# Performance work log

Hardware: AMD Instinct MI355X
Metric: run time of the kernel (lower is better)

## Reference

```python
import jax, jax.numpy as jnp
import numpy as np

# Dimensions (match init_kwargs / input_specs)
B, T, H, S, R, E = 4, 2048, 1024, 512, 16, 4
F = 6 + 2 * R           # engine_state_feature_dim
ETA = 0.1               # impression_rate
ACC_DECAY = 0.99        # accumulator EMA decay
EPS = 1e-6


def setup_inputs() -> dict:
    key = jax.random.key(0)
    ks = jax.random.split(key, 20)
    n = jax.random.normal
    x = n(ks[0], (B, T, H), jnp.float32)
    # ComplexLinear signal_proj: hidden -> state
    sig_Wr = n(ks[1], (H, S), jnp.float32) / np.sqrt(H).astype(np.float32)
    sig_Wi = n(ks[2], (H, S), jnp.float32) / np.sqrt(H).astype(np.float32)
    sig_br = jnp.zeros((S,), jnp.float32)
    sig_bi = jnp.zeros((S,), jnp.float32)
    # Per-engine complex state projection [E, S, R] and diagonal complex decay [E, R]
    A_r = n(ks[3], (E, S, R), jnp.float32) / np.sqrt(S).astype(np.float32)
    A_i = n(ks[4], (E, S, R), jnp.float32) / np.sqrt(S).astype(np.float32)
    mag = 0.90 + 0.09 * jax.random.uniform(ks[5], (E, R), jnp.float32)
    ph = (2.0 * np.pi) * jax.random.uniform(ks[6], (E, R), jnp.float32)
    lam_r = mag * jnp.cos(ph)
    lam_i = mag * jnp.sin(ph)
    # Per-engine ComplexLinear: feature(F) -> hidden(H)
    eh_Wr = n(ks[7], (E, F, H), jnp.float32) / np.sqrt(F).astype(np.float32)
    eh_Wi = n(ks[8], (E, F, H), jnp.float32) / np.sqrt(F).astype(np.float32)
    eh_br = jnp.zeros((E, H), jnp.float32)
    eh_bi = jnp.zeros((E, H), jnp.float32)
    # Engine fusion ComplexLinear: E*H -> H
    fu_Wr = n(ks[9], (E * H, H), jnp.float32) / np.sqrt(E * H).astype(np.float32)
    fu_Wi = n(ks[10], (E * H, H), jnp.float32) / np.sqrt(E * H).astype(np.float32)
    fu_br = jnp.zeros((H,), jnp.float32)
    fu_bi = jnp.zeros((H,), jnp.float32)
    # Gate: Linear(4H -> H)
    g_W = n(ks[11], (4 * H, H), jnp.float32) / np.sqrt(4 * H).astype(np.float32)
    g_b = jnp.zeros((H,), jnp.float32)
    return dict(x=x, sig_Wr=sig_Wr, sig_Wi=sig_Wi, sig_br=sig_br, sig_bi=sig_bi,
                A_r=A_r, A_i=A_i, lam_r=lam_r, lam_i=lam_i,
                eh_Wr=eh_Wr, eh_Wi=eh_Wi, eh_br=eh_br, eh_bi=eh_bi,
                fu_Wr=fu_Wr, fu_Wi=fu_Wi, fu_br=fu_br, fu_bi=fu_bi,
                g_W=g_W, g_b=g_b)


def _run_engines(ur, ui, lam_r, lam_i):
    """Complex diagonal recurrence over time for all engines jointly.
    ur, ui: [E,B,T,R] complex drive. Returns per-step features [E,B,T,F] (real, imag)."""
    lr = lam_r[:, None, :]  # [E,1,R]
    li = lam_i[:, None, :]

    def step(carry, u):
        hr, hi, acc = carry                      # [E,B,R], [E,B,R], [E,B]
        ur_t, ui_t = u                           # [E,B,R]
        nhr = (1.0 - ETA) * (lr * hr - li * hi) + ETA * ur_t
        nhi = (1.0 - ETA) * (lr * hi + li * hr) + ETA * ui_t
        mag2 = nhr * nhr + nhi * nhi             # [E,B,R]
        m_mean = jnp.mean(mag2, axis=-1)         # [E,B]
        nacc = ACC_DECAY * acc + (1.0 - ACC_DECAY) * m_mean
        inv = jax.lax.rsqrt(m_mean + EPS)[..., None]
        hnr, hni = nhr * inv, nhi * inv          # rms-normalized complex state
        z = jnp.zeros_like(m_mean)
        scal_r = jnp.stack([hnr.mean(-1), hni.mean(-1),
                            jnp.sqrt(m_mean + EPS),
                            jnp.sqrt(jnp.max(mag2, axis=-1) + EPS),
                            nacc, jnp.log1p(nacc)], axis=-1)   # [E,B,6]
        scal_i = jnp.stack([hni.mean(-1), -hnr.mean(-1), z, z, z, z], axis=-1)
        fr = jnp.concatenate([scal_r, hnr, hni], axis=-1)      # [E,B,F]
        fi = jnp.concatenate([scal_i, hni, -hnr], axis=-1)
        return (nhr, nhi, nacc), (fr, fi)

    init = (jnp.zeros((E, B, R), ur.dtype), jnp.zeros((E, B, R), ur.dtype),
            jnp.zeros((E, B), ur.dtype))
    u_seq = (jnp.moveaxis(ur, 2, 0), jnp.moveaxis(ui, 2, 0))   # [T,E,B,R]
    _, (frs, fis) = jax.lax.scan(step, init, u_seq)
    return jnp.moveaxis(frs, 0, 2), jnp.moveaxis(fis, 0, 2)    # [E,B,T,F]


def reference(x, sig_Wr, sig_Wi, sig_br, sig_bi, A_r, A_i, lam_r, lam_i,
              eh_Wr, eh_Wi, eh_br, eh_bi, fu_Wr, fu_Wi, fu_br, fu_bi, g_W, g_b):
    # Complex signal projection of real input: z = (Wr + i Wi)^T x + b
    zr = x @ sig_Wr + sig_br                     # [B,T,S]
    zi = x @ sig_Wi + sig_bi
    # Complex per-engine drive u = A^H-style complex matmul: [E,B,T,R]
    ur = jnp.einsum('bts,esr->ebtr', zr, A_r) - jnp.einsum('bts,esr->ebtr', zi, A_i)
    ui = jnp.einsum('bts,esr->ebtr', zr, A_i) + jnp.einsum('bts,esr->ebtr', zi, A_r)
    fr, fi = _run_engines(ur, ui, lam_r, lam_i)  # [E,B,T,F]
    # Per-engine ComplexLinear feature -> hidden
    yr = (jnp.einsum('ebtf,efh->ebth', fr, eh_Wr)
          - jnp.einsum('ebtf,efh->ebth', fi, eh_Wi)) + eh_br[:, None, None, :]
    yi = (jnp.einsum('ebtf,efh->ebth', fr, eh_Wi)
          + jnp.einsum('ebtf,efh->ebth', fi, eh_Wr)) + eh_bi[:, None, None, :]
    # Concat engines along feature axis -> [B,T,E*H]
    yr_c = jnp.moveaxis(yr, 0, 2).reshape(B, T, E * H)
    yi_c = jnp.moveaxis(yi, 0, 2).reshape(B, T, E * H)
    # Engine fusion ComplexLinear
    frf = yr_c @ fu_Wr - yi_c @ fu_Wi + fu_br    # [B,T,H]
    fif = yr_c @ fu_Wi + yi_c @ fu_Wr + fu_bi
    mag = jnp.sqrt(frf * frf + fif * fif + EPS)
    g = jax.nn.sigmoid(jnp.concatenate([x, frf, fif, mag], axis=-1) @ g_W + g_b)
    return g * frf + (1.0 - g) * x
```

## Files before the change

### kernel.cpp

```cpp
#include <hip/hip_runtime.h>
#include <stdint.h>

#define B_ 4
#define T_ 2048
#define H_ 1024
#define S_ 512
#define R_ 16
#define E_ 4
#define F_ 38
#define BT_ (B_*T_)
#define KF_ 320

typedef __attribute__((ext_vector_type(8))) __bf16 bf16x8;
typedef __attribute__((ext_vector_type(4))) float f32x4;

static __device__ __forceinline__ unsigned short f2bf(float f) {
    unsigned int u = __float_as_uint(f);
    unsigned int r = (u + 0x7fffu + ((u >> 16) & 1u)) >> 16;
    return (unsigned short)r;
}

__global__ __launch_bounds__(256) void k_gemm(
    const unsigned short* __restrict__ A, int lda,
    const unsigned short* __restrict__ BT, int ldb,
    float* __restrict__ C, int ldc,
    const float* __restrict__ bias, int K,
    size_t sA, size_t sB, size_t sC)
{
    A  += (size_t)blockIdx.z * sA;
    BT += (size_t)blockIdx.z * sB;
    C  += (size_t)blockIdx.z * sC;
    __shared__ unsigned short As[128 * 32];
    __shared__ unsigned short Bs[128 * 32];
    const int tid = threadIdx.x;
    const int l = tid & 63;
    const int w = tid >> 6;
    const int wm = w >> 1, wn = w & 1;
    const int m16 = l & 15, kg = l >> 4;
    const size_t bm = (size_t)blockIdx.y * 128;
    const size_t bn = (size_t)blockIdx.x * 128;

    const int rS = tid >> 2;
    const int kS = (tid & 3) * 8;
    const unsigned short* pA0 = A + (bm + rS) * (size_t)lda + kS;
    const unsigned short* pA1 = pA0 + (size_t)64 * lda;
    const unsigned short* pB0 = BT + (bn + rS) * (size_t)ldb + kS;
    const unsigned short* pB1 = pB0 + (size_t)64 * ldb;

    f32x4 acc[4][4];
#pragma unroll
    for (int i = 0; i < 4; ++i)
#pragma unroll
        for (int j = 0; j < 4; ++j) acc[i][j] = (f32x4){0.f, 0.f, 0.f, 0.f};

    uint4 ra0 = *(const uint4*)pA0;
    uint4 ra1 = *(const uint4*)pA1;
    uint4 rb0 = *(const uint4*)pB0;
    uint4 rb1 = *(const uint4*)pB1;

    const int s0 = tid * 8;
    const int s1 = (256 + tid) * 8;
    const int nkt = K >> 5;
    for (int kt = 0; kt < nkt; ++kt) {
        __syncthreads();
        *(uint4*)&As[s0] = ra0;
        *(uint4*)&As[s1] = ra1;
        *(uint4*)&Bs[s0] = rb0;
        *(uint4*)&Bs[s1] = rb1;
        if (kt + 1 < nkt) {
            pA0 += 32; pA1 += 32; pB0 += 32; pB1 += 32;
            ra0 = *(const uint4*)pA0;
            ra1 = *(const uint4*)pA1;
            rb0 = *(const uint4*)pB0;
            rb1 = *(const uint4*)pB1;
        }
        __syncthreads();
        bf16x8 af[4], bfr[4];
#pragma unroll
        for (int i = 0; i < 4; ++i)
            af[i] = *(const bf16x8*)&As[(wm * 64 + i * 16 + m16) * 32 + kg * 8];
#pragma unroll
        for (int j = 0; j < 4; ++j)
            bfr[j] = *(const bf16x8*)&Bs[(wn * 64 + j * 16 + m16) * 32 + kg * 8];
#pragma unroll
        for (int i = 0; i < 4; ++i)
#pragma unroll
            for (int j = 0; j < 4; ++j)
                acc[i][j] = __builtin_amdgcn_mfma_f32_16x16x32_bf16(af[i], bfr[j], acc[i][j], 0, 0, 0);
    }

#pragma unroll
    for (int j = 0; j < 4; ++j) {
        const size_t col = bn + wn * 64 + j * 16 + m16;
        const float bv = bias ? bias[col] : 0.f;
#pragma unroll
        for (int i = 0; i < 4; ++i) {
            const size_t row0 = bm + wm * 64 + i * 16 + kg * 4;
#pragma unroll
            for (int p = 0; p < 4; ++p)
                C[(row0 + p) * (size_t)ldc + col] = acc[i][j][p] + bv;
        }
    }
}

__global__ __launch_bounds__(256) void k_cast_x(const float* __restrict__ x,
                                                unsigned short* __restrict__ Abig)
{
    const int gid = blockIdx.x * 256 + threadIdx.x;
    const int row = gid >> 8;
    const int c4 = (gid & 255) << 2;
    float4 v = *(const float4*)&x[(size_t)row * H_ + c4];
    ushort4 o;
    o.x = f2bf(v.x); o.y = f2bf(v.y); o.z = f2bf(v.z); o.w = f2bf(v.w);
    *(ushort4*)&Abig[(size_t)row * 4096 + c4] = o;
}

__global__ __launch_bounds__(256) void k_gwt(const float* __restrict__ gW,
                                             unsigned short* __restrict__ gWT)
{
    __shared__ float tile[32][33];
    const int tx = threadIdx.x & 31, ty = threadIdx.x >> 5;
    const int k0 = blockIdx.x * 32, n0 = blockIdx.y * 32;
#pragma unroll
    for (int q = 0; q < 4; ++q) {
        int kk = ty * 4 + q;
        tile[kk][tx] = gW[(size_t)(k0 + kk) * H_ + n0 + tx];
    }
    __syncthreads();
#pragma unroll
    for (int q = 0; q < 4; ++q) {
        int nn = ty * 4 + q;
        gWT[(size_t)(n0 + nn) * 4096 + k0 + tx] = f2bf(tile[tx][nn]);
    }
}

__global__ __launch_bounds__(64) void k_wu(const float* __restrict__ sigWr,
                                           const float* __restrict__ sigWi,
                                           const float* __restrict__ A_r,
                                           const float* __restrict__ A_i,
                                           unsigned short* __restrict__ WuT)
{
    __shared__ float swr[S_], swi[S_];
    const int h = blockIdx.x;
    const int tid = threadIdx.x;
    for (int s = tid; s < S_; s += 64) {
        swr[s] = sigWr[(size_t)h * S_ + s];
        swi[s] = sigWi[(size_t)h * S_ + s];
    }
    __syncthreads();
    const int e = tid >> 4, r = tid & 15;
    float a0 = 0.f, a1 = 0.f;
    for (int s = 0; s < S_; ++s) {
        float ar = A_r[((size_t)(e * S_ + s)) * R_ + r];
        float ai = A_i[((size_t)(e * S_ + s)) * R_ + r];
        float wr = swr[s], wi = swi[s];
        a0 += wr * ar - wi * ai;
        a1 += wr * ai + wi * ar;
    }
    WuT[(size_t)tid * H_ + h] = f2bf(a0);
    WuT[(size_t)(64 + tid) * H_ + h] = f2bf(a1);
}

__global__ __launch_bounds__(64) void k_bu(const float* __restrict__ sigbr,
                                           const float* __restrict__ sigbi,
                                           const float* __restrict__ A_r,
                                           const float* __restrict__ A_i,
                                           float* __restrict__ b_u)
{
    const int n = blockIdx.x;
    const int lane = threadIdx.x;
    const int m = n & 63;
    const int e = m >> 4, r = m & 15;
    const bool hi = n >= 64;
    float acc = 0.f;
    for (int s = lane; s < S_; s += 64) {
        float ar = A_r[((size_t)(e * S_ + s)) * R_ + r];
        float ai = A_i[((size_t)(e * S_ + s)) * R_ + r];
        float br = sigbr[s], bi = sigbi[s];
        acc += hi ? (br * ai + bi * ar) : (br * ar - bi * ai);
    }
#pragma unroll
    for (int st = 32; st; st >>= 1) acc += __shfl_down(acc, st, 64);
    if (lane == 0) b_u[n] = acc;
}

__global__ __launch_bounds__(256) void k_prepA(const float* __restrict__ ehWr,
                                               const float* __restrict__ ehWi,
                                               const float* __restrict__ ehbr,
                                               const float* __restrict__ ehbi,
                                               unsigned short* __restrict__ Ac)
{
    const int gid = blockIdx.x * 256 + threadIdx.x;
    const int e = gid >> 16;
    const int rem = gid & 65535;
    const int row = rem >> 9;
    const int k = (rem & 511) << 2;
    float4 f = {0.f, 0.f, 0.f, 0.f};
    if (row < F_) {
        const float* src = (k < 1024) ? ehWr + ((size_t)(e * F_ + row)) * 1024 + k
                                      : ehWi + ((size_t)(e * F_ + row)) * 1024 + (k - 1024);
        f = *(const float4*)src;
    } else if (row == F_) {
        const float* src = (k < 1024) ? ehbr + (size_t)e * 1024 + k
                                      : ehbi + (size_t)e * 1024 + (k - 1024);
        f = *(const float4*)src;
    }
    ushort4 o;
    o.x = f2bf(f.x); o.y = f2bf(f.y); o.z = f2bf(f.z); o.w = f2bf(f.w);
    *(ushort4*)&Ac[(size_t)gid * 4] = o;
}

__global__ __launch_bounds__(256) void k_prepB(const float* __restrict__ fuWr,
                                               const float* __restrict__ fuWi,
                                               unsigned short* __restrict__ Bc)
{
    __shared__ float tR[32][33], tI[32][33];
    const int e = blockIdx.z;
    const int k0 = blockIdx.x * 32;
    const int h0 = blockIdx.y * 32;
    const int tx = threadIdx.x & 31, ty = threadIdx.x >> 5;
    const float* fr = fuWr + ((size_t)e * 1024 + k0) * 1024 + h0;
    const float* fi = fuWi + ((size_t)e * 1024 + k0) * 1024 + h0;
#pragma unroll
    for (int q = 0; q < 4; ++q) {
        int kk = ty * 4 + q;
        tR[kk][tx] = fr[(size_t)kk * 1024 + tx];
        tI[kk][tx] = fi[(size_t)kk * 1024 + tx];
    }
    __syncthreads();
    unsigned short* Be = Bc + (size_t)e * 2048 * 2048;
#pragma unroll
    for (int q = 0; q < 4; ++q) {
        int rr = ty * 4 + q;
        float vR = tR[tx][rr], vI = tI[tx][rr];
        size_t rowLo = (size_t)(h0 + rr) * 2048;
        size_t rowHi = (size_t)(1024 + h0 + rr) * 2048;
        Be[rowLo + k0 + tx]        = f2bf(vR);
        Be[rowLo + 1024 + k0 + tx] = f2bf(-vI);
        Be[rowHi + k0 + tx]        = f2bf(vI);
        Be[rowHi + 1024 + k0 + tx] = f2bf(vR);
    }
}

__global__ __launch_bounds__(256) void k_w2t(const float* __restrict__ C,
                                             unsigned short* __restrict__ W2T)
{
    const int gid = blockIdx.x * 256 + threadIdx.x;
    const int n = gid / KF_;
    const int k = gid - n * KF_;
    const int h = n & (H_ - 1);
    const bool hiRow = n >= H_;
    float v = 0.f;
    if (k < 304) {
        const int fp = (k < 152) ? k : k - 152;
        const int e = fp / F_;
        const int f = fp - e * F_;
        const float* Ce = C + ((size_t)e * 128 + f) * 2048;
        const float mr = Ce[h], mi = Ce[1024 + h];
        if (!hiRow) v = (k < 152) ? mr : -mi;
        else        v = (k < 152) ? mi :  mr;
    }
    W2T[gid] = f2bf(v);
}

__global__ __launch_bounds__(256) void k_b2(const float* __restrict__ fubr,
                                            const float* __restrict__ fubi,
                                            const float* __restrict__ C,
                                            float* __restrict__ b2)
{
    const int n = blockIdx.x * 256 + threadIdx.x;
    float v = (n < H_) ? fubr[n] : fubi[n - H_];
#pragma unroll
    for (int e = 0; e < 4; ++e)
        v += C[(size_t)e * 128 * 2048 + (size_t)F_ * 2048 + n];
    b2[n] = v;
}

__global__ __launch_bounds__(64) void k_scan(const float* __restrict__ U,
                                             const float* __restrict__ lam_r,
                                             const float* __restrict__ lam_i,
                                             float* __restrict__ Hr, float* __restrict__ Hi)
{
    const int wid = blockIdx.x;
    const int b = wid >> 6, ch = wid & 63;
    const int lane = threadIdx.x;
    const float cr = 0.9f * lam_r[ch];
    const float ci = 0.9f * lam_i[ch];
    const float* Ub = U + (size_t)b * T_ * 128;
    const int t0 = lane * 32;
    float ur[32], ui[32];
#pragma unroll
    for (int j = 0; j < 32; ++j) {
        ur[j] = Ub[(size_t)(t0 + j) * 128 + ch];
        ui[j] = Ub[(size_t)(t0 + j) * 128 + 64 + ch];
    }
    float hr = 0.f, hi = 0.f;
#pragma unroll
    for (int j = 0; j < 32; ++j) {
        float nr = fmaf(cr, hr, fmaf(-ci, hi, 0.1f * ur[j]));
        float ni = fmaf(cr, hi, fmaf(ci, hr, 0.1f * ui[j]));
        hr = nr; hi = ni;
    }
    float dr = cr, di = ci;
#pragma unroll
    for (int q = 0; q < 5; ++q) { float t = dr*dr - di*di; di = 2.f*dr*di; dr = t; }
    float xr = hr, xi = hi;
#pragma unroll
    for (int st = 1; st < 64; st <<= 1) {
        float yr = __shfl_up(xr, (unsigned)st, 64);
        float yi = __shfl_up(xi, (unsigned)st, 64);
        if (lane >= st) {
            float nxr = fmaf(dr, yr, fmaf(-di, yi, xr));
            float nxi = fmaf(dr, yi, fmaf(di, yr, xi));
            xr = nxr; xi = nxi;
        }
        float t = dr*dr - di*di; di = 2.f*dr*di; dr = t;
    }
    float ir = __shfl_up(xr, 1u, 64);
    float ii = __shfl_up(xi, 1u, 64);
    if (lane == 0) { ir = 0.f; ii = 0.f; }
    hr = ir; hi = ii;
    float* HrB = Hr + (size_t)b * T_ * 64;
    float* HiB = Hi + (size_t)b * T_ * 64;
#pragma unroll
    for (int j = 0; j < 32; ++j) {
        float nr = fmaf(cr, hr, fmaf(-ci, hi, 0.1f * ur[j]));
        float ni = fmaf(cr, hi, fmaf(ci, hr, 0.1f * ui[j]));
        HrB[(size_t)(t0 + j) * 64 + ch] = nr;
        HiB[(size_t)(t0 + j) * 64 + ch] = ni;
        hr = nr; hi = ni;
    }
}

__global__ __launch_bounds__(256) void k_feat(const float* __restrict__ Hr,
                                              const float* __restrict__ Hi,
                                              unsigned short* __restrict__ Fcat,
                                              float* __restrict__ Mbuf)
{
    const int gid = blockIdx.x * 256 + threadIdx.x;
    const int e = gid & 3;
    const int bt = gid >> 2;
    const float* hr = Hr + (size_t)bt * 64 + e * 16;
    const float* hi = Hi + (size_t)bt * 64 + e * 16;
    float nr[16], ni[16];
#pragma unroll
    for (int q = 0; q < 4; ++q) {
        float4 vr = ((const float4*)hr)[q];
        float4 vi = ((const float4*)hi)[q];
        nr[q*4+0]=vr.x; nr[q*4+1]=vr.y; nr[q*4+2]=vr.z; nr[q*4+3]=vr.w;
        ni[q*4+0]=vi.x; ni[q*4+1]=vi.y; ni[q*4+2]=vi.z; ni[q*4+3]=vi.w;
    }
    float sum = 0.f, mx = 0.f, sr = 0.f, si = 0.f;
#pragma unroll
    for (int i = 0; i < 16; ++i) {
        float m2 = nr[i] * nr[i] + ni[i] * ni[i];
        sum += m2; mx = fmaxf(mx, m2);
        sr += nr[i]; si += ni[i];
    }
    const float mm = sum * 0.0625f;
    const float inv = rsqrtf(mm + 1e-6f);
    const int b = bt >> 11, t = bt & (T_ - 1);
    Mbuf[(size_t)(e * 4 + b) * T_ + t] = mm;
    unsigned short* Fp = Fcat + (size_t)bt * KF_;
    const int br = e * F_, bi2 = 152 + e * F_;
    const float mhr = sr * 0.0625f * inv;
    const float mhi = si * 0.0625f * inv;
    Fp[br + 0] = f2bf(mhr);
    Fp[br + 1] = f2bf(mhi);
    Fp[br + 2] = f2bf(sqrtf(mm + 1e-6f));
    Fp[br + 3] = f2bf(sqrtf(mx + 1e-6f));
    Fp[bi2 + 0] = f2bf(mhi);
    Fp[bi2 + 1] = f2bf(-mhr);
#pragma unroll
    for (int i = 0; i < 16; ++i) {
        float a = nr[i] * inv, c = ni[i] * inv;
        Fp[br + 6 + i]   = f2bf(a);
        Fp[br + 22 + i]  = f2bf(c);
        Fp[bi2 + 6 + i]  = f2bf(c);
        Fp[bi2 + 22 + i] = f2bf(-a);
    }
}

__global__ __launch_bounds__(256) void k_acc(const float* __restrict__ Mbuf,
                                             unsigned short* __restrict__ Fcat)
{
    const int w = blockIdx.x * 4 + (threadIdx.x >> 6);
    const int lane = threadIdx.x & 63;
    const int e = w >> 2, b = w & 3;
    const float* mp = Mbuf + (size_t)(e * 4 + b) * T_ + lane * 32;
    float m[32];
#pragma unroll
    for (int j = 0; j < 32; ++j) m[j] = mp[j];
    float s = 0.f;
#pragma unroll
    for (int j = 0; j < 32; ++j) s = fmaf(0.99f, s, 0.01f * m[j]);
    float d = 0.99f;
#pragma unroll
    for (int q = 0; q < 5; ++q) d = d * d;
    float x = s;
#pragma unroll
    for (int st = 1; st < 64; st <<= 1) {
        float y = __shfl_up(x, (unsigned)st, 64);
        if (lane >= st) x = fmaf(d, y, x);
        d = d * d;
    }
    float init = __shfl_up(x, 1u, 64);
    if (lane == 0) init = 0.f;
    float acc = init;
#pragma unroll
    for (int j = 0; j < 32; ++j) {
        acc = fmaf(0.99f, acc, 0.01f * m[j]);
        const int t = lane * 32 + j;
        size_t ro = ((size_t)(b * T_ + t)) * KF_ + e * F_;
        Fcat[ro + 4] = f2bf(acc);
        Fcat[ro + 5] = f2bf(log1pf(acc));
    }
}

__global__ __launch_bounds__(256) void k_mag(const float* __restrict__ FRF,
                                             unsigned short* __restrict__ Abig)
{
    const int gid = blockIdx.x * 256 + threadIdx.x;
    const int row = gid >> 10;
    const int h = gid & (H_ - 1);
    const float fr = FRF[(size_t)row * 2048 + h];
    const float fi = FRF[(size_t)row * 2048 + 1024 + h];
    const size_t base = (size_t)row * 4096;
    Abig[base + 1024 + h] = f2bf(fr);
    Abig[base + 2048 + h] = f2bf(fi);
    Abig[base + 3072 + h] = f2bf(sqrtf(fr * fr + fi * fi + 1e-6f));
}

__global__ __launch_bounds__(256) void k_final(const float* __restrict__ preact,
                                               const float* __restrict__ gb,
                                               const float* __restrict__ FRF,
                                               const float* __restrict__ x,
                                               float* __restrict__ out)
{
    const int gid = blockIdx.x * 256 + threadIdx.x;
    const int h = gid & (H_ - 1);
    const int row = gid >> 10;
    const float z = preact[gid] + gb[h];
    const float g = 1.f / (1.f + __expf(-z));
    const float fr = FRF[(size_t)row * 2048 + h];
    out[gid] = g * fr + (1.f - g) * x[gid];
}

extern "C" void kernel_launch(void* const* d_in, const int* in_sizes, int n_in,
                              void* d_out, int out_size, void* d_ws, size_t ws_size,
                              hipStream_t stream)
{
    const float* x     = (const float*)d_in[0];
    const float* sigWr = (const float*)d_in[1];
    const float* sigWi = (const float*)d_in[2];
    const float* sigbr = (const float*)d_in[3];
    const float* sigbi = (const float*)d_in[4];
    const float* A_r   = (const float*)d_in[5];
    const float* A_i   = (const float*)d_in[6];
    const float* lam_r = (const float*)d_in[7];
    const float* lam_i = (const float*)d_in[8];
    const float* ehWr  = (const float*)d_in[9];
    const float* ehWi  = (const float*)d_in[10];
    const float* ehbr  = (const float*)d_in[11];
    const float* ehbi  = (const float*)d_in[12];
    const float* fuWr  = (const float*)d_in[13];
    const float* fuWi  = (const float*)d_in[14];
    const float* fubr  = (const float*)d_in[15];
    const float* fubi  = (const float*)d_in[16];
    const float* gW    = (const float*)d_in[17];
    const float* gb    = (const float*)d_in[18];

    char* ws = (char*)d_ws;
    size_t off = 0;
    auto alloc = [&](size_t bytes) -> void* {
        void* p = ws + off;
        off = (off + bytes + 255) & ~(size_t)255;
        return p;
    };
    unsigned short* Abig = (unsigned short*)alloc((size_t)BT_ * 4096 * 2);
    float* FRF           = (float*)alloc((size_t)BT_ * 2048 * 4);
    unsigned short* Fcat = (unsigned short*)alloc((size_t)BT_ * KF_ * 2);
    float* U             = (float*)alloc((size_t)BT_ * 128 * 4);
    float* Hr            = (float*)alloc((size_t)BT_ * 64 * 4);
    float* Hi            = (float*)alloc((size_t)BT_ * 64 * 4);
    float* Mbuf          = (float*)alloc((size_t)16 * T_ * 4);
    float* preact        = (float*)alloc((size_t)BT_ * H_ * 4);
    unsigned short* WuT  = (unsigned short*)alloc((size_t)128 * H_ * 2);
    float* b_u           = (float*)alloc(128 * 4);
    unsigned short* W2T  = (unsigned short*)alloc((size_t)2048 * KF_ * 2);
    float* b2            = (float*)alloc(2048 * 4);
    unsigned short* gWT  = (unsigned short*)alloc((size_t)H_ * 4096 * 2);
    unsigned short* Acomp= (unsigned short*)alloc((size_t)4 * 128 * 2048 * 2);
    unsigned short* Bcomp = (unsigned short*)FRF;
    float* Ccomp          = (float*)preact;
    if (off > ws_size) return;

    hipMemsetAsync(Fcat, 0, (size_t)BT_ * KF_ * 2, stream);

    k_cast_x<<<dim3(BT_ * H_ / 4 / 256), dim3(256), 0, stream>>>(x, Abig);
    k_gwt<<<dim3(128, 32), dim3(256), 0, stream>>>(gW, gWT);
    k_wu<<<dim3(H_), dim3(64), 0, stream>>>(sigWr, sigWi, A_r, A_i, WuT);
    k_bu<<<dim3(128), dim3(64), 0, stream>>>(sigbr, sigbi, A_r, A_i, b_u);
    k_prepA<<<dim3(1024), dim3(256), 0, stream>>>(ehWr, ehWi, ehbr, ehbi, Acomp);
    k_prepB<<<dim3(32, 32, 4), dim3(256), 0, stream>>>(fuWr, fuWi, Bcomp);

    k_gemm<<<dim3(16, 1, 4), dim3(256), 0, stream>>>(
        Acomp, 2048, Bcomp, 2048, Ccomp, 2048, (const float*)nullptr, 2048,
        (size_t)128 * 2048, (size_t)2048 * 2048, (size_t)128 * 2048);

    k_w2t<<<dim3(2048 * KF_ / 256), dim3(256), 0, stream>>>(Ccomp, W2T);
    k_b2<<<dim3(8), dim3(256), 0, stream>>>(fubr, fubi, Ccomp, b2);

    k_gemm<<<dim3(1, 64), dim3(256), 0, stream>>>(Abig, 4096, WuT, H_, U, 128, b_u, H_, 0, 0, 0);

    k_scan<<<dim3(B_ * 64), dim3(64), 0, stream>>>(U, lam_r, lam_i, Hr, Hi);
    k_feat<<<dim3(BT_ * E_ / 256), dim3(256), 0, stream>>>(Hr, Hi, Fcat, Mbuf);
    k_acc<<<dim3(4), dim3(256), 0, stream>>>(Mbuf, Fcat);

    k_gemm<<<dim3(16, 64), dim3(256), 0, stream>>>(Fcat, KF_, W2T, KF_, FRF, 2048, b2, KF_, 0, 0, 0);

    k_mag<<<dim3(BT_ * H_ / 256), dim3(256), 0, stream>>>(FRF, Abig);

    k_gemm<<<dim3(8, 64), dim3(256), 0, stream>>>(Abig, 4096, gWT, 4096, preact, H_, (const float*)nullptr, 4096, 0, 0, 0);

    k_final<<<dim3(BT_ * H_ / 256), dim3(256), 0, stream>>>(preact, gb, FRF, x, (float*)d_out);
}
```

Measured before the change: 354.4 us.

## Fuse magnitude and gating epilogues into GEMMs, use direct-to-LDS loads and split-K

The GEMM kernel is templated with four epilogues. The fusion GEMM now writes interleaved real/imag columns, converts them to bf16 and computes the magnitude in place, which removes the k_mag kernel. The gate GEMM applies the sigmoid blend directly, which removes k_final and the preact buffer. The drive GEMM is split-K over 4 slices with atomicAdd onto a bias-initialised U. Tile loads now go straight from global memory to LDS through global_load_lds, with a second barrier per k-step, and workgroups are remapped to group neighbouring tiles. In exchange the kernel gives up register double-buffering, adds atomics, and allocates separate workspace for Bcomp and Ccomp.

```diff
diff --git a/kernel.cpp b/kernel.cpp
--- a/kernel.cpp
+++ b/kernel.cpp
@@ -20,32 +20,59 @@
     return (unsigned short)r;
 }
 
+static __device__ __forceinline__ void gload_lds16(const unsigned short* g, unsigned short* l) {
+    __builtin_amdgcn_global_load_lds(
+        (const __attribute__((address_space(1))) unsigned int*)g,
+        (__attribute__((address_space(3))) unsigned int*)l, 16, 0, 0);
+}
+
+template<int EPI>
 __global__ __launch_bounds__(256) void k_gemm(
     const unsigned short* __restrict__ A, int lda,
     const unsigned short* __restrict__ BT, int ldb,
     float* __restrict__ C, int ldc,
     const float* __restrict__ bias, int K,
-    size_t sA, size_t sB, size_t sC)
+    size_t sA, size_t sB, size_t sC, int nbx,
+    const float* __restrict__ aux1, const float* __restrict__ aux2,
+    unsigned short* __restrict__ auxO)
 {
     A  += (size_t)blockIdx.z * sA;
     BT += (size_t)blockIdx.z * sB;
     C  += (size_t)blockIdx.z * sC;
+
+    int bx, by;
+    {
+        const int f = blockIdx.x;
+        const int nwg = gridDim.x;
+        int s;
+        if ((nwg & 7) == 0) {
+            const int q = nwg >> 3;
+            s = (f & 7) * q + (f >> 3);
+        } else s = f;
+        by = s / nbx; bx = s - by * nbx;
+    }
+
     __shared__ unsigned short As[128 * 32];
     __shared__ unsigned short Bs[128 * 32];
     const int tid = threadIdx.x;
     const int l = tid & 63;
-    const int w = tid >> 6;
-    const int wm = w >> 1, wn = w & 1;
+    const int wv = tid >> 6;
+    const int wm = wv >> 1, wn = wv & 1;
     const int m16 = l & 15, kg = l >> 4;
-    const size_t bm = (size_t)blockIdx.y * 128;
-    const size_t bn = (size_t)blockIdx.x * 128;
-
-    const int rS = tid >> 2;
-    const int kS = (tid & 3) * 8;
-    const unsigned short* pA0 = A + (bm + rS) * (size_t)lda + kS;
-    const unsigned short* pA1 = pA0 + (size_t)64 * lda;
-    const unsigned short* pB0 = BT + (bn + rS) * (size_t)ldb + kS;
-    const unsigned short* pB1 = pB0 + (size_t)64 * ldb;
+    const size_t bm = (size_t)by * 128;
+    const size_t bn = (size_t)bx * 128;
+
+    const int slab0 = wv * 2, slab1 = wv * 2 + 1;
+    const int rIn = l >> 2;
+    const int kOff = (l & 3) * 8;
+    const unsigned short* gA0 = A + (bm + slab0 * 16 + rIn) * (size_t)lda + kOff;
+    const unsigned short* gA1 = A + (bm + slab1 * 16 + rIn) * (size_t)lda + kOff;
+    const unsigned short* gB0 = BT + (bn + slab0 * 16 + rIn) * (size_t)ldb + kOff;
+    const unsigned short* gB1 = BT + (bn + slab1 * 16 + rIn) * (size_t)ldb + kOff;
+    unsigned short* lA0 = As + slab0 * 512;
+    unsigned short* lA1 = As + slab1 * 512;
+    unsigned short* lB0 = Bs + slab0 * 512;
+    unsigned short* lB1 = Bs + slab1 * 512;
 
     f32x4 acc[4][4];
 #pragma unroll
@@ -53,27 +80,13 @@
 #pragma unroll
         for (int j = 0; j < 4; ++j) acc[i][j] = (f32x4){0.f, 0.f, 0.f, 0.f};
 
-    uint4 ra0 = *(const uint4*)pA0;
-    uint4 ra1 = *(const uint4*)pA1;
-    uint4 rb0 = *(const uint4*)pB0;
-    uint4 rb1 = *(const uint4*)pB1;
-
-    const int s0 = tid * 8;
-    const int s1 = (256 + tid) * 8;
     const int nkt = K >> 5;
     for (int kt = 0; kt < nkt; ++kt) {
-        __syncthreads();
-        *(uint4*)&As[s0] = ra0;
-        *(uint4*)&As[s1] = ra1;
-        *(uint4*)&Bs[s0] = rb0;
-        *(uint4*)&Bs[s1] = rb1;
-        if (kt + 1 < nkt) {
-            pA0 += 32; pA1 += 32; pB0 += 32; pB1 += 32;
-            ra0 = *(const uint4*)pA0;
-            ra1 = *(const uint4*)pA1;
-            rb0 = *(const uint4*)pB0;
-            rb1 = *(const uint4*)pB1;
-        }
+        gload_lds16(gA0, lA0);
+        gload_lds16(gA1, lA1);
+        gload_lds16(gB0, lB0);
+        gload_lds16(gB1, lB1);
+        gA0 += 32; gA1 += 32; gB0 += 32; gB1 += 32;
         __syncthreads();
         bf16x8 af[4], bfr[4];
 #pragma unroll
@@ -87,18 +100,42 @@
 #pragma unroll
             for (int j = 0; j < 4; ++j)
                 acc[i][j] = __builtin_amdgcn_mfma_f32_16x16x32_bf16(af[i], bfr[j], acc[i][j], 0, 0, 0);
+        __syncthreads();
     }
 
 #pragma unroll
     for (int j = 0; j < 4; ++j) {
         const size_t col = bn + wn * 64 + j * 16 + m16;
-        const float bv = bias ? bias[col] : 0.f;
+        const float bv = (EPI == 1) ? 0.f : (bias ? bias[col] : 0.f);
 #pragma unroll
         for (int i = 0; i < 4; ++i) {
             const size_t row0 = bm + wm * 64 + i * 16 + kg * 4;
 #pragma unroll
-            for (int p = 0; p < 4; ++p)
-                C[(row0 + p) * (size_t)ldc + col] = acc[i][j][p] + bv;
+            for (int p = 0; p < 4; ++p) {
+                const size_t row = row0 + p;
+                if constexpr (EPI == 0) {
+                    C[row * (size_t)ldc + col] = acc[i][j][p] + bv;
+                } else if constexpr (EPI == 1) {
+                    atomicAdd(&C[row * (size_t)ldc + col], acc[i][j][p]);
+                } else if constexpr (EPI == 2) {
+                    const float v = acc[i][j][p] + bv;
+                    const float w = __shfl_xor(v, 1, 64);
+                    const int h = (int)(col >> 1);
+                    if ((col & 1) == 0) {
+                        C[row * 1024 + h] = v;
+                        auxO[row * 4096 + 1024 + h] = f2bf(v);
+                    } else {
+                        auxO[row * 4096 + 2048 + h] = f2bf(v);
+                        auxO[row * 4096 + 3072 + h] = f2bf(sqrtf(w * w + v * v + 1e-6f));
+                    }
+                } else {
+                    const float z = acc[i][j][p] + bv;
+                    const float g = 1.f / (1.f + __expf(-z));
+                    const float fr = aux1[row * 1024 + col];
+                    const float xv = aux2[row * 1024 + col];
+                    C[row * 1024 + col] = fmaf(g, fr - xv, xv);
+                }
+            }
         }
     }
 }
@@ -182,6 +219,13 @@
 #pragma unroll
     for (int st = 32; st; st >>= 1) acc += __shfl_down(acc, st, 64);
     if (lane == 0) b_u[n] = acc;
+}
+
+__global__ __launch_bounds__(256) void k_uinit(const float* __restrict__ b_u,
+                                               float* __restrict__ U)
+{
+    const int gid = blockIdx.x * 256 + threadIdx.x;
+    U[gid] = b_u[gid & 127];
 }
 
 __global__ __launch_bounds__(256) void k_prepA(const float* __restrict__ ehWr,
@@ -248,8 +292,8 @@
     const int gid = blockIdx.x * 256 + threadIdx.x;
     const int n = gid / KF_;
     const int k = gid - n * KF_;
-    const int h = n & (H_ - 1);
-    const bool hiRow = n >= H_;
+    const int h = n >> 1;
+    const int s = n & 1;
     float v = 0.f;
     if (k < 304) {
         const int fp = (k < 152) ? k : k - 152;
@@ -257,7 +301,7 @@
         const int f = fp - e * F_;
         const float* Ce = C + ((size_t)e * 128 + f) * 2048;
         const float mr = Ce[h], mi = Ce[1024 + h];
-        if (!hiRow) v = (k < 152) ? mr : -mi;
+        if (s == 0) v = (k < 152) ? mr : -mi;
         else        v = (k < 152) ? mi :  mr;
     }
     W2T[gid] = f2bf(v);
@@ -269,10 +313,13 @@
                                             float* __restrict__ b2)
 {
     const int n = blockIdx.x * 256 + threadIdx.x;
-    float v = (n < H_) ? fubr[n] : fubi[n - H_];
+    const int h = n >> 1;
+    const int s = n & 1;
+    const int colOld = s * 1024 + h;
+    float v = s ? fubi[h] : fubr[h];
 #pragma unroll
     for (int e = 0; e < 4; ++e)
-        v += C[(size_t)e * 128 * 2048 + (size_t)F_ * 2048 + n];
+        v += C[(size_t)e * 128 * 2048 + (size_t)F_ * 2048 + colOld];
     b2[n] = v;
 }
 
@@ -415,35 +462,6 @@
         Fcat[ro + 4] = f2bf(acc);
         Fcat[ro + 5] = f2bf(log1pf(acc));
     }
-}
-
-__global__ __launch_bounds__(256) void k_mag(const float* __restrict__ FRF,
-                                             unsigned short* __restrict__ Abig)
-{
-    const int gid = blockIdx.x * 256 + threadIdx.x;
-    const int row = gid >> 10;
-    const int h = gid & (H_ - 1);
-    const float fr = FRF[(size_t)row * 2048 + h];
-    const float fi = FRF[(size_t)row * 2048 + 1024 + h];
-    const size_t base = (size_t)row * 4096;
-    Abig[base + 1024 + h] = f2bf(fr);
-    Abig[base + 2048 + h] = f2bf(fi);
-    Abig[base + 3072 + h] = f2bf(sqrtf(fr * fr + fi * fi + 1e-6f));
-}
-
-__global__ __launch_bounds__(256) void k_final(const float* __restrict__ preact,
-                                               const float* __restrict__ gb,
-                                               const float* __restrict__ FRF,
-                                               const float* __restrict__ x,
-                                               float* __restrict__ out)
-{
-    const int gid = blockIdx.x * 256 + threadIdx.x;
-    const int h = gid & (H_ - 1);
-    const int row = gid >> 10;
-    const float z = preact[gid] + gb[h];
-    const float g = 1.f / (1.f + __expf(-z));
-    const float fr = FRF[(size_t)row * 2048 + h];
-    out[gid] = g * fr + (1.f - g) * x[gid];
 }
 
 extern "C" void kernel_launch(void* const* d_in, const int* in_sizes, int n_in,
@@ -478,21 +496,20 @@
         return p;
     };
     unsigned short* Abig = (unsigned short*)alloc((size_t)BT_ * 4096 * 2);
-    float* FRF           = (float*)alloc((size_t)BT_ * 2048 * 4);
+    float* FRFr          = (float*)alloc((size_t)BT_ * 1024 * 4);
     unsigned short* Fcat = (unsigned short*)alloc((size_t)BT_ * KF_ * 2);
     float* U             = (float*)alloc((size_t)BT_ * 128 * 4);
     float* Hr            = (float*)alloc((size_t)BT_ * 64 * 4);
     float* Hi            = (float*)alloc((size_t)BT_ * 64 * 4);
     float* Mbuf          = (float*)alloc((size_t)16 * T_ * 4);
-    float* preact        = (float*)alloc((size_t)BT_ * H_ * 4);
     unsigned short* WuT  = (unsigned short*)alloc((size_t)128 * H_ * 2);
     float* b_u           = (float*)alloc(128 * 4);
     unsigned short* W2T  = (unsigned short*)alloc((size_t)2048 * KF_ * 2);
     float* b2            = (float*)alloc(2048 * 4);
     unsigned short* gWT  = (unsigned short*)alloc((size_t)H_ * 4096 * 2);
     unsigned short* Acomp= (unsigned short*)alloc((size_t)4 * 128 * 2048 * 2);
-    unsigned short* Bcomp = (unsigned short*)FRF;
-    float* Ccomp          = (float*)preact;
+    unsigned short* Bcomp= (unsigned short*)alloc((size_t)4 * 2048 * 2048 * 2);
+    float* Ccomp         = (float*)alloc((size_t)4 * 128 * 2048 * 4);
     if (off > ws_size) return;
 
     hipMemsetAsync(Fcat, 0, (size_t)BT_ * KF_ * 2, stream);
@@ -504,24 +521,28 @@
     k_prepA<<<dim3(1024), dim3(256), 0, stream>>>(ehWr, ehWi, ehbr, ehbi, Acomp);
     k_prepB<<<dim3(32, 32, 4), dim3(256), 0, stream>>>(fuWr, fuWi, Bcomp);
 
-    k_gemm<<<dim3(16, 1, 4), dim3(256), 0, stream>>>(
+    k_gemm<0><<<dim3(16, 1, 4), dim3(256), 0, stream>>>(
         Acomp, 2048, Bcomp, 2048, Ccomp, 2048, (const float*)nullptr, 2048,
-        (size_t)128 * 2048, (size_t)2048 * 2048, (size_t)128 * 2048);
+        (size_t)128 * 2048, (size_t)2048 * 2048, (size_t)128 * 2048, 16,
+        nullptr, nullptr, nullptr);
 
     k_w2t<<<dim3(2048 * KF_ / 256), dim3(256), 0, stream>>>(Ccomp, W2T);
     k_b2<<<dim3(8), dim3(256), 0, stream>>>(fubr, fubi, Ccomp, b2);
 
-    k_gemm<<<dim3(1, 64), dim3(256), 0, stream>>>(Abig, 4096, WuT, H_, U, 128, b_u, H_, 0, 0, 0);
+    k_uinit<<<dim3(BT_ * 128 / 256), dim3(256), 0, stream>>>(b_u, U);
+    k_gemm<1><<<dim3(64, 1, 4), dim3(256), 0, stream>>>(
+        Abig, 4096, WuT, H_, U, 128, (const float*)nullptr, 256,
+        (size_t)256, (size_t)256, (size_t)0, 1, nullptr, nullptr, nullptr);
 
     k_scan<<<dim3(B_ * 64), dim3(64), 0, stream>>>(U, lam_r, lam_i, Hr, Hi);
     k_feat<<<dim3(BT_ * E_ / 256), dim3(256), 0, stream>>>(Hr, Hi, Fcat, Mbuf);
     k_acc<<<dim3(4), dim3(256), 0, stream>>>(Mbuf, Fcat);
 
-    k_gemm<<<dim3(16, 64), dim3(256), 0, stream>>>(Fcat, KF_, W2T, KF_, FRF, 2048, b2, KF_, 0, 0, 0);
-
-    k_mag<<<dim3(BT_ * H_ / 256), dim3(256), 0, stream>>>(FRF, Abig);
-
-    k_gemm<<<dim3(8, 64), dim3(256), 0, stream>>>(Abig, 4096, gWT, 4096, preact, H_, (const float*)nullptr, 4096, 0, 0, 0);
-
-    k_final<<<dim3(BT_ * H_ / 256), dim3(256), 0, stream>>>(preact, gb, FRF, x, (float*)d_out);
-}
+    k_gemm<2><<<dim3(1024, 1, 1), dim3(256), 0, stream>>>(
+        Fcat, KF_, W2T, KF_, FRFr, 1024, b2, KF_,
+        (size_t)0, (size_t)0, (size_t)0, 16, nullptr, nullptr, Abig);
+
+    k_gemm<3><<<dim3(512, 1, 1), dim3(256), 0, stream>>>(
+        Abig, 4096, gWT, 4096, (float*)d_out, 1024, gb, 4096,
+        (size_t)0, (size_t)0, (size_t)0, 8, FRFr, x, nullptr);
+}
```

Result: slower. 412.3 us (+16.3%).
